# Performance work log

Measured on AMD Instinct MI355X. Metric: run time of the kernel, lower is better.

Reference implementation:

```python
import jax, jax.numpy as jnp
import numpy as np

N_E = 8192
E_DIM = 256
BETA = 0.25


def setup_inputs() -> dict:
    key = jax.random.key(0)
    k1, k2 = jax.random.split(key)
    z = jax.random.normal(k1, (16, 256, 32, 32), dtype=jnp.float32)
    # embedding.weight.data.uniform_(-1/n_e, 1/n_e)
    emb = jax.random.uniform(k2, (N_E, E_DIM), dtype=jnp.float32,
                             minval=-1.0 / N_E, maxval=1.0 / N_E)
    return {"z": z, "emb": emb}


def reference(z, emb):
    # z: (B, C, H, W) with C == e_dim
    zp = jnp.transpose(z, (0, 2, 3, 1))            # (B, H, W, C)
    zf = zp.reshape(-1, emb.shape[1])              # (N, e_dim)
    # squared-distance matrix: ||z||^2 + ||e||^2 - 2 z.e
    d = (jnp.sum(zf * zf, axis=1, keepdims=True)
         + jnp.sum(emb * emb, axis=1)
         - 2.0 * zf @ emb.T)                       # (N, n_e)
    idx = jnp.argmin(d, axis=1)                    # (N,)
    # one-hot @ weight is just a gather
    z_q = emb[idx].reshape(zp.shape)               # (B, H, W, C)
    sg = jax.lax.stop_gradient
    loss = jnp.mean((sg(z_q) - zp) ** 2) + BETA * jnp.mean((z_q - sg(zp)) ** 2)
    # straight-through estimator
    z_q = zp + sg(z_q - zp)
    z_q = jnp.transpose(z_q, (0, 3, 1, 2))         # (B, C, H, W)
    return z_q, loss
```

## Files before the change

### kernel.cpp

```cpp
#include <hip/hip_runtime.h>
#include <hip/hip_bf16.h>

#define EDIM 256
#define NE   8192
#define HW   1024
#define NTOK 16384
#define TOT  (16*EDIM*HW)
#define NSEG 16
#define TPB  32
#define ESC  16384.0f
#define SC1  0x7F7F7F7F

typedef __attribute__((ext_vector_type(8))) int  int8v;
typedef __attribute__((ext_vector_type(4))) int  int4v;
typedef __attribute__((ext_vector_type(4))) float f32x4;
typedef unsigned long long u64;

#define KEY_OFF   0
#define ACC_OFF   131072
#define CNT_OFF   131076
#define ZF_OFF    131584
#define EMBB_OFF  (ZF_OFF + 4194304)

__device__ __forceinline__ ushort f2bf(float f) {
    __hip_bfloat16 h = __float2bfloat16(f);
    return *reinterpret_cast<ushort*>(&h);
}

__device__ __forceinline__ uint f4fp8(float a, float b, float c, float d) {
    uint r = __builtin_amdgcn_cvt_pk_fp8_f32(a, b, 0, false);
    r = __builtin_amdgcn_cvt_pk_fp8_f32(c, d, r, true);
    return r;
}

__device__ __forceinline__ void gl16(const void* g, void* l) {
    __builtin_amdgcn_global_load_lds(
        (const __attribute__((address_space(1))) void*)g,
        (__attribute__((address_space(3))) void*)l, 16, 0, 0);
}

__global__ __launch_bounds__(256) void k_prep(const float* __restrict__ z,
                                              const float* __restrict__ emb,
                                              uchar* __restrict__ zf,
                                              uchar* __restrict__ embB,
                                              u64* __restrict__ key64,
                                              float* __restrict__ acc,
                                              uint* __restrict__ cnt) {
    __shared__ float ldsf[64][68];
    int bid = blockIdx.x;
    int t = threadIdx.x;
    if (bid < 1024) {
        int ct = bid & 3, hwt = (bid >> 2) & 15, b = bid >> 6;
        int c0 = ct * 64, hw0 = hwt * 64;
        int hq = (t & 15) * 4;
        int rw = t >> 4;
#pragma unroll
        for (int i = 0; i < 4; i++) {
            int cl = i * 16 + rw;
            float4 v = *reinterpret_cast<const float4*>(
                z + (size_t)(b * EDIM + c0 + cl) * HW + hw0 + hq);
            *reinterpret_cast<float4*>(&ldsf[cl][hq]) = v;
        }
        __syncthreads();
        int c4 = (t & 15) * 4;
#pragma unroll
        for (int i = 0; i < 4; i++) {
            int r = i * 16 + (t >> 4);
            float4 v = *reinterpret_cast<const float4*>(&ldsf[r][c4]);
            uint p = f4fp8(v.x, v.y, v.z, v.w);
            *reinterpret_cast<uint*>(zf + ((size_t)(b * HW + hw0 + r)) * EDIM + c0 + c4) = p;
        }
    } else {
        if (t < 8) key64[(bid - 1024) * 8 + t] = 0ull;
        if (bid == 1024) {
            if (t == 64) *acc = 0.f;
            if (t == 65) *cnt = 0u;
        }
        int row = (bid - 1024) * 4 + (t >> 6);
        int l = t & 63;
        float4 v = *reinterpret_cast<const float4*>(emb + row * EDIM + l * 4);
        uint p = f4fp8(v.x * ESC, v.y * ESC, v.z * ESC, v.w * ESC);
        int tile = row >> 4, arow = row & 15;
        int kh = l >> 5, kq = (l >> 3) & 3;
        int jh = (l >> 2) & 1, jl = (l & 3) * 4;
        *reinterpret_cast<uint*>(embB + tile * 4096 + kh * 2048 + jh * 1024 +
                                 (kq * 16 + arow) * 16 + jl) = p;
    }
}

#define TILE_COMPUTE(B0, B1, TGLOB) do {                                              \
    f32x4 ac0, ac1, ac2, ac3;                                                         \
    __builtin_amdgcn_s_setprio(1);                                                    \
    ac0 = __builtin_amdgcn_mfma_scale_f32_16x16x128_f8f6f4(a[0][0], B0, cz, 0, 0, 0, SC1, 0, SC1); \
    ac1 = __builtin_amdgcn_mfma_scale_f32_16x16x128_f8f6f4(a[1][0], B0, cz, 0, 0, 0, SC1, 0, SC1); \
    ac2 = __builtin_amdgcn_mfma_scale_f32_16x16x128_f8f6f4(a[2][0], B0, cz, 0, 0, 0, SC1, 0, SC1); \
    ac3 = __builtin_amdgcn_mfma_scale_f32_16x16x128_f8f6f4(a[3][0], B0, cz, 0, 0, 0, SC1, 0, SC1); \
    ac0 = __builtin_amdgcn_mfma_scale_f32_16x16x128_f8f6f4(a[0][1], B1, ac0, 0, 0, 0, SC1, 0, SC1); \
    ac1 = __builtin_amdgcn_mfma_scale_f32_16x16x128_f8f6f4(a[1][1], B1, ac1, 0, 0, 0, SC1, 0, SC1); \
    ac2 = __builtin_amdgcn_mfma_scale_f32_16x16x128_f8f6f4(a[2][1], B1, ac2, 0, 0, 0, SC1, 0, SC1); \
    ac3 = __builtin_amdgcn_mfma_scale_f32_16x16x128_f8f6f4(a[3][1], B1, ac3, 0, 0, 0, SC1, 0, SC1); \
    __builtin_amdgcn_s_setprio(0);                                                    \
    uint tgc = 511u - (uint)(TGLOB);                                                  \
    _Pragma("unroll")                                                                 \
    for (int r = 0; r < 4; r++) {                                                     \
        bvv[0][r] = fmaxf(bvv[0][r], __uint_as_float((__float_as_uint(ac0[r]) & 0xFFFFFE00u) | tgc)); \
        bvv[1][r] = fmaxf(bvv[1][r], __uint_as_float((__float_as_uint(ac1[r]) & 0xFFFFFE00u) | tgc)); \
        bvv[2][r] = fmaxf(bvv[2][r], __uint_as_float((__float_as_uint(ac2[r]) & 0xFFFFFE00u) | tgc)); \
        bvv[3][r] = fmaxf(bvv[3][r], __uint_as_float((__float_as_uint(ac3[r]) & 0xFFFFFE00u) | tgc)); \
    }                                                                                 \
} while (0)

__global__ __launch_bounds__(64, 4) void k_dist(const uchar* __restrict__ zf,
                                                const uchar* __restrict__ embB,
                                                u64* __restrict__ key64) {
    __shared__ __align__(16) uchar lbuf[2][4096];
    int bid = blockIdx.x;
    int rb = bid >> 4;
    int cs = bid & 15;
    int lane = threadIdx.x;
    int arow = lane & 15, kq = lane >> 4;
    int r0 = rb * 64;

    int8v a[4][2];
#pragma unroll
    for (int g = 0; g < 4; g++)
#pragma unroll
        for (int kh = 0; kh < 2; kh++)
            a[g][kh] = *reinterpret_cast<const int8v*>(
                zf + ((size_t)(r0 + g * 16 + arow)) * EDIM + kh * 128 + kq * 32);

    const uchar* tb = embB + (size_t)(cs * TPB) * 4096;
    uchar* myl = &lbuf[0][0];

    float bvv[4][4];
#pragma unroll
    for (int g = 0; g < 4; g++)
#pragma unroll
        for (int r = 0; r < 4; r++) bvv[g][r] = -3.4e38f;

    const f32x4 cz = {0.f, 0.f, 0.f, 0.f};

#pragma unroll
    for (int q = 0; q < 4; q++)
        gl16(tb + q * 1024 + lane * 16, myl + q * 1024);

    int tg0 = cs * TPB;
    for (int t = 0; t < TPB; ++t) {
        if (t + 1 < TPB) {
            const uchar* g = tb + (size_t)(t + 1) * 4096 + lane * 16;
            uchar* d = myl + ((t + 1) & 1) * 4096;
#pragma unroll
            for (int q = 0; q < 4; q++)
                gl16(g + q * 1024, d + q * 1024);
            asm volatile("s_waitcnt vmcnt(4)" ::: "memory");
        } else {
            asm volatile("s_waitcnt vmcnt(0)" ::: "memory");
        }
        const uchar* lp = myl + (t & 1) * 4096;
        int4v l0 = *reinterpret_cast<const int4v*>(lp + lane * 16);
        int4v h0 = *reinterpret_cast<const int4v*>(lp + 1024 + lane * 16);
        int4v l1 = *reinterpret_cast<const int4v*>(lp + 2048 + lane * 16);
        int4v h1 = *reinterpret_cast<const int4v*>(lp + 3072 + lane * 16);
        int8v b0 = __builtin_shufflevector(l0, h0, 0, 1, 2, 3, 4, 5, 6, 7);
        int8v b1 = __builtin_shufflevector(l1, h1, 0, 1, 2, 3, 4, 5, 6, 7);
        TILE_COMPUTE(b0, b1, tg0 + t);
    }

#pragma unroll
    for (int g = 0; g < 4; g++)
#pragma unroll
        for (int r = 0; r < 4; r++) {
            float v = bvv[g][r];
            int tg = 511 - (int)(__float_as_uint(v) & 0x1FFu);
            int i = tg * 16 + arow;
#pragma unroll
            for (int off = 1; off < 16; off <<= 1) {
                float v2 = __shfl_xor(v, off);
                int i2 = __shfl_xor(i, off);
                if (v2 > v || (v2 == v && i2 < i)) { v = v2; i = i2; }
            }
            if (arow == 0) {
                int row = r0 + g * 16 + kq * 4 + r;
                uint b = __float_as_uint(v);
                uint k32 = (b & 0x80000000u) ? ~b : (b | 0x80000000u);
                u64 key = ((u64)k32 << 32) | (u64)(uint)(8191 - i);
                atomicMax(&key64[row], key);
            }
        }
}

__global__ __launch_bounds__(256) void k_out(const float* __restrict__ z,
                                             const float* __restrict__ emb,
                                             const u64* __restrict__ key64,
                                             float* __restrict__ out,
                                             float* __restrict__ acc,
                                             uint* __restrict__ cnt) {
    __shared__ ushort eb[64][130];
    __shared__ int sidx[64];
    __shared__ float wsum[4];
    int t = threadIdx.x;
    int h = blockIdx.x & 1;
    int n0 = (blockIdx.x >> 1) * 64;
    int b = n0 >> 10;
    int hw0 = n0 & 1023;

    if (t < 64) sidx[t] = 8191 - (int)(uint)(key64[n0 + t] & 0xFFFFFFFFull);
    __syncthreads();

    {
        int r = t >> 2, part = t & 3;
        int j = sidx[r];
        const float* src = emb + (size_t)j * EDIM + h * 128 + part * 32;
#pragma unroll
        for (int i = 0; i < 8; i++) {
            float4 v = *reinterpret_cast<const float4*>(src + i * 4);
            ushort2 u0 = make_ushort2(f2bf(v.x), f2bf(v.y));
            ushort2 u1 = make_ushort2(f2bf(v.z), f2bf(v.w));
            *reinterpret_cast<ushort2*>(&eb[r][part * 32 + i * 4]) = u0;
            *reinterpret_cast<ushort2*>(&eb[r][part * 32 + i * 4 + 2]) = u1;
        }
    }
    __syncthreads();

    int hq = (t & 15) * 4;
    int c0l = (t >> 4) * 8;
    float ls = 0.f;
#pragma unroll
    for (int ci = 0; ci < 8; ci++) {
        int cl = c0l + ci;
        int cg = h * 128 + cl;
        size_t off = ((size_t)b * EDIM + cg) * HW + hw0 + hq;
        float4 zv = *reinterpret_cast<const float4*>(z + off);
        float e0 = __uint_as_float((uint)eb[hq + 0][cl] << 16);
        float e1 = __uint_as_float((uint)eb[hq + 1][cl] << 16);
        float e2 = __uint_as_float((uint)eb[hq + 2][cl] << 16);
        float e3 = __uint_as_float((uint)eb[hq + 3][cl] << 16);
        float d0 = e0 - zv.x, d1 = e1 - zv.y, d2 = e2 - zv.z, d3 = e3 - zv.w;
        ls += d0 * d0 + d1 * d1 + d2 * d2 + d3 * d3;
        *reinterpret_cast<float4*>(out + off) = make_float4(e0, e1, e2, e3);
    }

    int lane = t & 63, wid = t >> 6;
#pragma unroll
    for (int off = 32; off; off >>= 1) ls += __shfl_down(ls, off);
    if (lane == 0) wsum[wid] = ls;
    __syncthreads();
    if (t == 0) {
        atomicAdd(acc, wsum[0] + wsum[1] + wsum[2] + wsum[3]);
        __threadfence();
        uint old = atomicAdd(cnt, 1u);
        if (old == gridDim.x - 1) {
            float tot = atomicAdd(acc, 0.0f);
            out[TOT] = 1.25f * tot / (float)TOT;
        }
    }
}

extern "C" void kernel_launch(void* const* d_in, const int* in_sizes, int n_in,
                              void* d_out, int out_size, void* d_ws, size_t ws_size,
                              hipStream_t stream) {
    const float* z = (const float*)d_in[0];
    const float* emb = (const float*)d_in[1];
    float* out = (float*)d_out;
    char* ws = (char*)d_ws;

    u64*   key64 = (u64*)(ws + KEY_OFF);
    float* acc   = (float*)(ws + ACC_OFF);
    uint*  cnt   = (uint*)(ws + CNT_OFF);
    uchar* zf    = (uchar*)(ws + ZF_OFF);
    uchar* embB  = (uchar*)(ws + EMBB_OFF);

    k_prep<<<3072, 256, 0, stream>>>(z, emb, zf, embB, key64, acc, cnt);
    k_dist<<<4096, 64, 0, stream>>>(zf, embB, key64);
    k_out<<<512, 256, 0, stream>>>(z, emb, key64, out, acc, cnt);
}
```

Baseline: 82.98 us.

## Quantize distance GEMM operands to FP4 and swizzle prep transpose LDS

Switches the nearest-codebook search from FP8 to FP4 (e2m1) operands. It uses a custom round-to-nearest quantizer, halves the zf and embedding buffers, and runs the scaled MFMA in FP4 mode. This cuts global/LDS traffic and may raise MFMA throughput, but sharply lowers distance precision, so argmin picks may differ from the reference. The z transpose in the prep kernel also gets an XOR swizzle to avoid LDS bank conflicts.

```diff
diff --git a/kernel.cpp b/kernel.cpp
--- a/kernel.cpp
+++ b/kernel.cpp
@@ -8,7 +8,7 @@
 #define TOT  (16*EDIM*HW)
 #define NSEG 16
 #define TPB  32
-#define ESC  16384.0f
+#define ESC  32768.0f
 #define SC1  0x7F7F7F7F
 
 typedef __attribute__((ext_vector_type(8))) int  int8v;
@@ -16,21 +16,28 @@
 typedef __attribute__((ext_vector_type(4))) float f32x4;
 typedef unsigned long long u64;
 
+#define DUP8(x) __builtin_shufflevector(x, x, 0, 1, 2, 3, 0, 1, 2, 3)
+
 #define KEY_OFF   0
 #define ACC_OFF   131072
 #define CNT_OFF   131076
 #define ZF_OFF    131584
-#define EMBB_OFF  (ZF_OFF + 4194304)
+#define EMBB_OFF  (ZF_OFF + 2097152)
 
 __device__ __forceinline__ ushort f2bf(float f) {
     __hip_bfloat16 h = __float2bfloat16(f);
     return *reinterpret_cast<ushort*>(&h);
 }
 
-__device__ __forceinline__ uint f4fp8(float a, float b, float c, float d) {
-    uint r = __builtin_amdgcn_cvt_pk_fp8_f32(a, b, 0, false);
-    r = __builtin_amdgcn_cvt_pk_fp8_f32(c, d, r, true);
-    return r;
+__device__ __forceinline__ uint q4(float v) {
+    uint s = v < 0.f ? 8u : 0u;
+    float m = fabsf(v);
+    uint c = (m >= 0.25f) + (m >= 0.75f) + (m >= 1.25f) + (m >= 1.75f)
+           + (m >= 2.5f) + (m >= 3.5f) + (m >= 5.0f);
+    return s | c;
+}
+__device__ __forceinline__ ushort q4x4(float a, float b, float c, float d) {
+    return (ushort)(q4(a) | (q4(b) << 4) | (q4(c) << 8) | (q4(d) << 12));
 }
 
 __device__ __forceinline__ void gl16(const void* g, void* l) {
@@ -59,16 +66,19 @@
             int cl = i * 16 + rw;
             float4 v = *reinterpret_cast<const float4*>(
                 z + (size_t)(b * EDIM + c0 + cl) * HW + hw0 + hq);
-            *reinterpret_cast<float4*>(&ldsf[cl][hq]) = v;
+            int sc = ((hq >> 2) ^ (cl & 15)) << 2;
+            *reinterpret_cast<float4*>(&ldsf[cl][sc]) = v;
         }
         __syncthreads();
         int c4 = (t & 15) * 4;
 #pragma unroll
         for (int i = 0; i < 4; i++) {
             int r = i * 16 + (t >> 4);
-            float4 v = *reinterpret_cast<const float4*>(&ldsf[r][c4]);
-            uint p = f4fp8(v.x, v.y, v.z, v.w);
-            *reinterpret_cast<uint*>(zf + ((size_t)(b * HW + hw0 + r)) * EDIM + c0 + c4) = p;
+            int sc = ((c4 >> 2) ^ (r & 15)) << 2;
+            float4 v = *reinterpret_cast<const float4*>(&ldsf[r][sc]);
+            ushort p = q4x4(v.x, v.y, v.z, v.w);
+            *reinterpret_cast<ushort*>(zf + (size_t)(b * HW + hw0 + r) * 128 +
+                                       ((c0 + c4) >> 1)) = p;
         }
     } else {
         if (t < 8) key64[(bid - 1024) * 8 + t] = 0ull;
@@ -79,26 +89,26 @@
         int row = (bid - 1024) * 4 + (t >> 6);
         int l = t & 63;
         float4 v = *reinterpret_cast<const float4*>(emb + row * EDIM + l * 4);
-        uint p = f4fp8(v.x * ESC, v.y * ESC, v.z * ESC, v.w * ESC);
+        ushort p = q4x4(v.x * ESC, v.y * ESC, v.z * ESC, v.w * ESC);
         int tile = row >> 4, arow = row & 15;
-        int kh = l >> 5, kq = (l >> 3) & 3;
-        int jh = (l >> 2) & 1, jl = (l & 3) * 4;
-        *reinterpret_cast<uint*>(embB + tile * 4096 + kh * 2048 + jh * 1024 +
-                                 (kq * 16 + arow) * 16 + jl) = p;
-    }
-}
-
-#define TILE_COMPUTE(B0, B1, TGLOB) do {                                              \
+        int kh = l >> 5, kq = (l >> 3) & 3, jb = (l & 7) * 2;
+        *reinterpret_cast<ushort*>(embB + tile * 2048 + kh * 1024 +
+                                   (kq * 16 + arow) * 16 + jb) = p;
+    }
+}
+
+#define TILE_COMPUTE(B0L, B1L, TGLOB) do {                                            \
+    int8v B0 = DUP8(B0L), B1 = DUP8(B1L);                                             \
     f32x4 ac0, ac1, ac2, ac3;                                                         \
     __builtin_amdgcn_s_setprio(1);                                                    \
-    ac0 = __builtin_amdgcn_mfma_scale_f32_16x16x128_f8f6f4(a[0][0], B0, cz, 0, 0, 0, SC1, 0, SC1); \
-    ac1 = __builtin_amdgcn_mfma_scale_f32_16x16x128_f8f6f4(a[1][0], B0, cz, 0, 0, 0, SC1, 0, SC1); \
-    ac2 = __builtin_amdgcn_mfma_scale_f32_16x16x128_f8f6f4(a[2][0], B0, cz, 0, 0, 0, SC1, 0, SC1); \
-    ac3 = __builtin_amdgcn_mfma_scale_f32_16x16x128_f8f6f4(a[3][0], B0, cz, 0, 0, 0, SC1, 0, SC1); \
-    ac0 = __builtin_amdgcn_mfma_scale_f32_16x16x128_f8f6f4(a[0][1], B1, ac0, 0, 0, 0, SC1, 0, SC1); \
-    ac1 = __builtin_amdgcn_mfma_scale_f32_16x16x128_f8f6f4(a[1][1], B1, ac1, 0, 0, 0, SC1, 0, SC1); \
-    ac2 = __builtin_amdgcn_mfma_scale_f32_16x16x128_f8f6f4(a[2][1], B1, ac2, 0, 0, 0, SC1, 0, SC1); \
-    ac3 = __builtin_amdgcn_mfma_scale_f32_16x16x128_f8f6f4(a[3][1], B1, ac3, 0, 0, 0, SC1, 0, SC1); \
+    ac0 = __builtin_amdgcn_mfma_scale_f32_16x16x128_f8f6f4(DUP8(a[0][0]), B0, cz, 4, 4, 0, SC1, 0, SC1); \
+    ac1 = __builtin_amdgcn_mfma_scale_f32_16x16x128_f8f6f4(DUP8(a[1][0]), B0, cz, 4, 4, 0, SC1, 0, SC1); \
+    ac2 = __builtin_amdgcn_mfma_scale_f32_16x16x128_f8f6f4(DUP8(a[2][0]), B0, cz, 4, 4, 0, SC1, 0, SC1); \
+    ac3 = __builtin_amdgcn_mfma_scale_f32_16x16x128_f8f6f4(DUP8(a[3][0]), B0, cz, 4, 4, 0, SC1, 0, SC1); \
+    ac0 = __builtin_amdgcn_mfma_scale_f32_16x16x128_f8f6f4(DUP8(a[0][1]), B1, ac0, 4, 4, 0, SC1, 0, SC1); \
+    ac1 = __builtin_amdgcn_mfma_scale_f32_16x16x128_f8f6f4(DUP8(a[1][1]), B1, ac1, 4, 4, 0, SC1, 0, SC1); \
+    ac2 = __builtin_amdgcn_mfma_scale_f32_16x16x128_f8f6f4(DUP8(a[2][1]), B1, ac2, 4, 4, 0, SC1, 0, SC1); \
+    ac3 = __builtin_amdgcn_mfma_scale_f32_16x16x128_f8f6f4(DUP8(a[3][1]), B1, ac3, 4, 4, 0, SC1, 0, SC1); \
     __builtin_amdgcn_s_setprio(0);                                                    \
     uint tgc = 511u - (uint)(TGLOB);                                                  \
     _Pragma("unroll")                                                                 \
@@ -113,7 +123,7 @@
 __global__ __launch_bounds__(64, 4) void k_dist(const uchar* __restrict__ zf,
                                                 const uchar* __restrict__ embB,
                                                 u64* __restrict__ key64) {
-    __shared__ __align__(16) uchar lbuf[2][4096];
+    __shared__ __align__(16) uchar lbuf[2][2048];
     int bid = blockIdx.x;
     int rb = bid >> 4;
     int cs = bid & 15;
@@ -121,15 +131,15 @@
     int arow = lane & 15, kq = lane >> 4;
     int r0 = rb * 64;
 
-    int8v a[4][2];
+    int4v a[4][2];
 #pragma unroll
     for (int g = 0; g < 4; g++)
 #pragma unroll
         for (int kh = 0; kh < 2; kh++)
-            a[g][kh] = *reinterpret_cast<const int8v*>(
-                zf + ((size_t)(r0 + g * 16 + arow)) * EDIM + kh * 128 + kq * 32);
-
-    const uchar* tb = embB + (size_t)(cs * TPB) * 4096;
+            a[g][kh] = *reinterpret_cast<const int4v*>(
+                zf + ((size_t)(r0 + g * 16 + arow)) * 128 + kh * 64 + kq * 16);
+
+    const uchar* tb = embB + (size_t)(cs * TPB) * 2048;
     uchar* myl = &lbuf[0][0];
 
     float bvv[4][4];
@@ -141,28 +151,24 @@
     const f32x4 cz = {0.f, 0.f, 0.f, 0.f};
 
 #pragma unroll
-    for (int q = 0; q < 4; q++)
+    for (int q = 0; q < 2; q++)
         gl16(tb + q * 1024 + lane * 16, myl + q * 1024);
 
     int tg0 = cs * TPB;
     for (int t = 0; t < TPB; ++t) {
         if (t + 1 < TPB) {
-            const uchar* g = tb + (size_t)(t + 1) * 4096 + lane * 16;
-            uchar* d = myl + ((t + 1) & 1) * 4096;
-#pragma unroll
-            for (int q = 0; q < 4; q++)
+            const uchar* g = tb + (size_t)(t + 1) * 2048 + lane * 16;
+            uchar* d = myl + ((t + 1) & 1) * 2048;
+#pragma unroll
+            for (int q = 0; q < 2; q++)
                 gl16(g + q * 1024, d + q * 1024);
-            asm volatile("s_waitcnt vmcnt(4)" ::: "memory");
+            asm volatile("s_waitcnt vmcnt(2)" ::: "memory");
         } else {
             asm volatile("s_waitcnt vmcnt(0)" ::: "memory");
         }
-        const uchar* lp = myl + (t & 1) * 4096;
-        int4v l0 = *reinterpret_cast<const int4v*>(lp + lane * 16);
-        int4v h0 = *reinterpret_cast<const int4v*>(lp + 1024 + lane * 16);
-        int4v l1 = *reinterpret_cast<const int4v*>(lp + 2048 + lane * 16);
-        int4v h1 = *reinterpret_cast<const int4v*>(lp + 3072 + lane * 16);
-        int8v b0 = __builtin_shufflevector(l0, h0, 0, 1, 2, 3, 4, 5, 6, 7);
-        int8v b1 = __builtin_shufflevector(l1, h1, 0, 1, 2, 3, 4, 5, 6, 7);
+        const uchar* lp = myl + (t & 1) * 2048;
+        int4v b0 = *reinterpret_cast<const int4v*>(lp + lane * 16);
+        int4v b1 = *reinterpret_cast<const int4v*>(lp + 1024 + lane * 16);
         TILE_COMPUTE(b0, b1, tg0 + t);
     }
 
```

Result: faster. 80.30 us (-3.2%).
